# Optimization experiments

Hardware: AMD Instinct MI355X
Metric: run time of the kernel (lower is better)

Reference implementation:

```python
import jax, jax.numpy as jnp
import numpy as np

B, T, N = 256, 512, 128
GO, EOS = 1, 2  # mead-baseline Offsets
NEG = -10000.0


def setup_inputs() -> dict:
    key = jax.random.key(0)
    k1, k2, k3 = jax.random.split(key, 3)
    unaries = jax.random.normal(k1, (B, T, N), dtype=jnp.float32)
    # constraint mask: True where transition is INVALID (masked to -1e4)
    cmask = jax.random.bernoulli(k2, 0.3, (1, N, N))
    trans = jax.nn.log_softmax(
        jnp.where(cmask, jnp.float32(NEG), jnp.float32(0.0)), axis=1
    )  # [1, N, N], matches buffer construction in __init__
    lengths = jax.random.randint(k3, (B,), T // 2, T + 1).astype(jnp.int64)
    lengths = lengths.at[0].set(T)  # ensure max(lengths) == T
    return {"unaries": unaries, "trans": trans, "lengths": lengths}


def _viterbi(probv, trans, lengths, start_idx, end_idx):
    # probv: [T, B, N] log-probs; trans: [1, N, N]; lengths: [B]
    seq_len, batch, n_tags = probv.shape
    trans0 = trans[0]  # [N(cur), N(prev)]
    lengths = lengths.astype(jnp.int32)

    alphas = jnp.full((batch, n_tags), NEG, probv.dtype).at[:, start_idx].set(0.0)
    alphas = jax.nn.log_softmax(alphas, axis=-1)

    def step(alphas, xs):
        unary_t, i = xs  # [B, N], scalar
        ntv = alphas[:, None, :] + trans0[None]          # [B, N_cur, N_prev]
        bp = jnp.argmax(ntv, axis=2)                     # backpointers [B, N]
        new_alphas = jnp.max(ntv, axis=2) + unary_t      # [B, N]
        alphas = jnp.where((i < lengths)[:, None], new_alphas, alphas)
        return alphas, bp

    alphas, bps = jax.lax.scan(step, alphas, (probv, jnp.arange(seq_len)))

    terminal = alphas + trans0[end_idx][None, :]         # [B, N]
    path_score = jnp.max(terminal, axis=1)               # [B]
    best_tag = jnp.argmax(terminal, axis=1)              # [B]

    rev_len = seq_len - lengths - 1

    def back(btid, xs):
        bp, i = xs  # bp: [B, N]
        new = jnp.take_along_axis(bp, btid[:, None], axis=1)[:, 0]
        btid = jnp.where(i > rev_len, new, btid)
        return btid, btid

    _, ys = jax.lax.scan(back, best_tag, (bps[::-1], jnp.arange(seq_len)))
    full = jnp.concatenate([best_tag[None], ys], axis=0)  # [T+1, B]
    best_path = full[:seq_len][::-1]                       # [T, B]

    seq_mask = jnp.arange(seq_len)[:, None] < lengths[None, :]  # [T, B]
    best_path = jnp.where(seq_mask, best_path, 0)
    return best_path, path_score


def reference(unaries, trans, lengths):
    # constrained branch of TaggerGreedyDecoder.forward (batch_first=True)
    probv = jax.nn.log_softmax(jnp.swapaxes(unaries, 0, 1), axis=-1)  # [T,B,N]
    preds_tb, scores = _viterbi(probv, trans, lengths, GO, EOS)
    return jnp.swapaxes(preds_tb, 0, 1), scores  # ([B,T], [B])
```

## Files before the change

kernel.cpp:

```cpp
#include <hip/hip_runtime.h>

#define BB 256
#define TT 512
#define NN 128
#define GO_IDX 1
#define EOS_IDX 2
#define TSPLIT 496
#define NEGV (-10000.0f)
#define ASLOT(x) ((x) + (((x) >> 5) << 2))

__device__ __forceinline__ float dpp_xor1_f(float x) {
    return __int_as_float(__builtin_amdgcn_update_dpp(0, __float_as_int(x), 0xB1, 0xF, 0xF, true));
}
__device__ __forceinline__ float dpp_xor2_f(float x) {
    return __int_as_float(__builtin_amdgcn_update_dpp(0, __float_as_int(x), 0x4E, 0xF, 0xF, true));
}
__device__ __forceinline__ int dpp_xor1_i(int x) {
    return __builtin_amdgcn_update_dpp(0, x, 0xB1, 0xF, 0xF, true);
}
__device__ __forceinline__ int dpp_xor2_i(int x) {
    return __builtin_amdgcn_update_dpp(0, x, 0x4E, 0xF, 0xF, true);
}

__global__ __launch_bounds__(256) void lsm_kernel(float* __restrict__ u) {
    const int g0 = (blockIdx.x * 256 + threadIdx.x) >> 5;
    const int l  = threadIdx.x & 31;
    const int NG = 2048 * 8;
    float4* base = (float4*)u;
    int row = g0;
    float4 v = base[(size_t)row * 32 + l];
#pragma unroll
    for (int it = 0; it < 8; ++it) {
        const int nrow = row + NG;
        float4 vn = make_float4(0.f, 0.f, 0.f, 0.f);
        if (it < 7) vn = base[(size_t)nrow * 32 + l];
        float m = fmaxf(fmaxf(v.x, v.y), fmaxf(v.z, v.w));
#pragma unroll
        for (int off = 16; off; off >>= 1) m = fmaxf(m, __shfl_xor(m, off, 64));
        float s = expf(v.x - m) + expf(v.y - m) + expf(v.z - m) + expf(v.w - m);
#pragma unroll
        for (int off = 16; off; off >>= 1) s += __shfl_xor(s, off, 64);
        float ls = logf(s);
        base[(size_t)row * 32 + l] =
            make_float4((v.x - m) - ls, (v.y - m) - ls, (v.z - m) - ls, (v.w - m) - ls);
        v = vn; row = nrow;
    }
}

__global__ __launch_bounds__(512) void viterbi_kernel(
    const float* __restrict__ probs,
    const float* __restrict__ trans,
    const int*   __restrict__ lengths_raw,
    float* __restrict__ out,
    unsigned char* __restrict__ ws)
{
    __shared__ unsigned char bps[(TSPLIT - 1) * NN];
    __shared__ __align__(16) float alpha[2][144];
    __shared__ float fin_v[2];
    __shared__ int   fin_i[2];

    const int tid  = threadIdx.x;
    const int b    = blockIdx.x;
    const int wave = tid >> 6;
    const int lane = tid & 63;
    const int q    = tid & 3;
    const int cur  = tid >> 2;

    int len;
    {
        int probe = lengths_raw[1];
        len = (probe == 0) ? lengths_raw[2 * b] : lengths_raw[b];
    }

    float tr[32];
    {
        const float4* t4 = (const float4*)(trans + cur * NN + q * 32);
#pragma unroll
        for (int i = 0; i < 8; ++i) {
            float4 v = t4[i];
            tr[4*i+0] = v.x; tr[4*i+1] = v.y; tr[4*i+2] = v.z; tr[4*i+3] = v.w;
        }
    }

    if (tid < NN) alpha[0][ASLOT(tid)] = (tid == GO_IDX) ? 0.0f : NEGV;

    const float* pb = probs + (size_t)b * TT * NN;
    unsigned char* wst = ws + (size_t)b * ((TT - TSPLIT) * NN);

    float P[8], Nx[8];
    if (q == 0) {
#pragma unroll
        for (int k = 0; k < 8; ++k) P[k] = pb[k * NN + cur];
    }
    __syncthreads();

    const int nG = (len + 7) >> 3;
    for (int g = 0; g < nG; ++g) {
        const int tb = g * 8;
        if (q == 0) {
#pragma unroll
            for (int k = 0; k < 8; ++k) {
                int tt = tb + 8 + k; if (tt > TT - 1) tt = TT - 1;
                Nx[k] = pb[tt * NN + cur];
            }
        }
#pragma unroll
        for (int k = 0; k < 8; ++k) {
            const int t = tb + k;
            if (t < len) {
                const float* ra = alpha[t & 1];
                float*       wa = alpha[(t & 1) ^ 1];
                const float4* a4 = (const float4*)(ra + q * 36);
                float bv[4]; int bi[4];
#pragma unroll
                for (int c = 0; c < 4; ++c) {
                    float4 a0 = a4[c * 2], a1 = a4[c * 2 + 1];
                    const int base = c * 8;
                    bv[c] = a0.x + tr[base + 0]; bi[c] = base + 0;
                    float x;
                    x = a0.y + tr[base + 1]; if (x > bv[c]) { bv[c] = x; bi[c] = base + 1; }
                    x = a0.z + tr[base + 2]; if (x > bv[c]) { bv[c] = x; bi[c] = base + 2; }
                    x = a0.w + tr[base + 3]; if (x > bv[c]) { bv[c] = x; bi[c] = base + 3; }
                    x = a1.x + tr[base + 4]; if (x > bv[c]) { bv[c] = x; bi[c] = base + 4; }
                    x = a1.y + tr[base + 5]; if (x > bv[c]) { bv[c] = x; bi[c] = base + 5; }
                    x = a1.z + tr[base + 6]; if (x > bv[c]) { bv[c] = x; bi[c] = base + 6; }
                    x = a1.w + tr[base + 7]; if (x > bv[c]) { bv[c] = x; bi[c] = base + 7; }
                }
                float best = bv[0]; int bp = bi[0];
#pragma unroll
                for (int c = 1; c < 4; ++c) { if (bv[c] > best) { best = bv[c]; bp = bi[c]; } }
                bp += q * 32;

                float v1 = dpp_xor1_f(best); int b1 = dpp_xor1_i(bp);
                bool  t1 = (q & 1) ? (v1 >= best) : (v1 > best);
                float m1 = t1 ? v1 : best;   int p1 = t1 ? b1 : bp;
                float v2 = dpp_xor2_f(m1);   int b2 = dpp_xor2_i(p1);
                bool  t2 = (q & 2) ? (v2 >= m1) : (v2 > m1);
                float M  = t2 ? v2 : m1;     int BP = t2 ? b2 : p1;

                if (q == 0) {
                    wa[ASLOT(cur)] = M + P[k];
                    if (t >= 1) {
                        if (t < TSPLIT) bps[(t - 1) * NN + cur] = (unsigned char)BP;
                        else            wst[(t - TSPLIT) * NN + cur] = (unsigned char)BP;
                    }
                }
                __syncthreads();
            }
        }
#pragma unroll
        for (int k = 0; k < 8; ++k) P[k] = Nx[k];
    }

    __threadfence();

    if (tid < NN) {
        float v = alpha[len & 1][ASLOT(tid)] + trans[EOS_IDX * NN + tid];
        int idx = tid;
#pragma unroll
        for (int off = 32; off; off >>= 1) {
            float ov = __shfl_xor(v, off, 64);
            int   oi = __shfl_xor(idx, off, 64);
            if (ov > v || (ov == v && oi < idx)) { v = ov; idx = oi; }
        }
        if (lane == 0) { fin_v[wave] = v; fin_i[wave] = idx; }
    }
    __syncthreads();

    for (int t = len + tid; t < TT; t += 512) out[(size_t)b * TT + t] = 0.0f;

    if (tid == 0) {
        float v0 = fin_v[0], v1 = fin_v[1];
        int   i0 = fin_i[0], i1 = fin_i[1];
        float sc; int tag;
        if (v1 > v0) { sc = v1; tag = i1; }
        else         { sc = v0; tag = i0; }
        out[(size_t)BB * TT + b] = sc;

        for (int t = len - 1; t >= 0; --t) {
            out[(size_t)b * TT + t] = (float)tag;
            if (t >= 1) {
                int nb;
                if (t < TSPLIT) nb = bps[(t - 1) * NN + tag];
                else            nb = ((volatile const unsigned char*)wst)[(t - TSPLIT) * NN + tag];
                tag = nb;
            }
        }
    }
}

extern "C" void kernel_launch(void* const* d_in, const int* in_sizes, int n_in,
                              void* d_out, int out_size, void* d_ws, size_t ws_size,
                              hipStream_t stream) {
    float*       unaries = (float*)d_in[0];
    const float* trans   = (const float*)d_in[1];
    const int*   lengths = (const int*)d_in[2];
    float* out = (float*)d_out;
    unsigned char* ws = (unsigned char*)d_ws;

    hipLaunchKernelGGL(lsm_kernel, dim3(2048), dim3(256), 0, stream, unaries);
    hipLaunchKernelGGL(viterbi_kernel, dim3(BB), dim3(512), 0, stream,
                       unaries, trans, lengths, out, ws);
}
```

Measured before the change: 508.6 us.

## Skip log-softmax past sequence length and use lighter per-step barrier

The log-softmax kernel now maps each block to one batch and only normalizes rows below that batch's length, because the Viterbi pass never reads later timesteps. This removes memory traffic for padded rows. Separately, the per-timestep __syncthreads in the Viterbi recurrence is replaced by an inline-asm LDS waitcnt plus s_barrier. That drops the wait on outstanding global/vmem operations but relies on the asm memory clobber for correct ordering.

```diff
diff --git a/kernel.cpp b/kernel.cpp
--- a/kernel.cpp
+++ b/kernel.cpp
@@ -9,6 +9,8 @@
 #define NEGV (-10000.0f)
 #define ASLOT(x) ((x) + (((x) >> 5) << 2))
 
+#define STEP_BARRIER() asm volatile("s_waitcnt lgkmcnt(0)\n\ts_barrier" ::: "memory")
+
 __device__ __forceinline__ float dpp_xor1_f(float x) {
     return __int_as_float(__builtin_amdgcn_update_dpp(0, __float_as_int(x), 0xB1, 0xF, 0xF, true));
 }
@@ -22,18 +24,25 @@
     return __builtin_amdgcn_update_dpp(0, x, 0x4E, 0xF, 0xF, true);
 }
 
-__global__ __launch_bounds__(256) void lsm_kernel(float* __restrict__ u) {
+__global__ __launch_bounds__(256) void lsm_kernel(float* __restrict__ u,
+                                                  const int* __restrict__ lengths_raw) {
     const int g0 = (blockIdx.x * 256 + threadIdx.x) >> 5;
     const int l  = threadIdx.x & 31;
-    const int NG = 2048 * 8;
-    float4* base = (float4*)u;
-    int row = g0;
-    float4 v = base[(size_t)row * 32 + l];
-#pragma unroll
-    for (int it = 0; it < 8; ++it) {
-        const int nrow = row + NG;
-        float4 vn = make_float4(0.f, 0.f, 0.f, 0.f);
-        if (it < 7) vn = base[(size_t)nrow * 32 + l];
+    const int b  = g0 >> 6;
+    const int j  = g0 & 63;
+    int len;
+    {
+        int probe = lengths_raw[1];
+        len = (probe == 0) ? lengths_raw[2 * b] : lengths_raw[b];
+    }
+    float4* base = (float4*)(u + (size_t)b * TT * NN);
+    int row = j;
+    float4 v = base[row * 32 + l];
+    for (;;) {
+        const int nrow = row + 64;
+        const bool more = (nrow < len);
+        float4 vn;
+        if (more) vn = base[nrow * 32 + l];
         float m = fmaxf(fmaxf(v.x, v.y), fmaxf(v.z, v.w));
 #pragma unroll
         for (int off = 16; off; off >>= 1) m = fmaxf(m, __shfl_xor(m, off, 64));
@@ -41,8 +50,9 @@
 #pragma unroll
         for (int off = 16; off; off >>= 1) s += __shfl_xor(s, off, 64);
         float ls = logf(s);
-        base[(size_t)row * 32 + l] =
+        base[row * 32 + l] =
             make_float4((v.x - m) - ls, (v.y - m) - ls, (v.z - m) - ls, (v.w - m) - ls);
+        if (!more) break;
         v = vn; row = nrow;
     }
 }
@@ -145,7 +155,7 @@
                         else            wst[(t - TSPLIT) * NN + cur] = (unsigned char)BP;
                     }
                 }
-                __syncthreads();
+                STEP_BARRIER();
             }
         }
 #pragma unroll
@@ -198,7 +208,7 @@
     float* out = (float*)d_out;
     unsigned char* ws = (unsigned char*)d_ws;
 
-    hipLaunchKernelGGL(lsm_kernel, dim3(2048), dim3(256), 0, stream, unaries);
+    hipLaunchKernelGGL(lsm_kernel, dim3(2048), dim3(256), 0, stream, unaries, lengths);
     hipLaunchKernelGGL(viterbi_kernel, dim3(BB), dim3(512), 0, stream,
                        unaries, trans, lengths, out, ws);
 }
```

After: 507.1 us. No clear change (-0.3%).
